# Optimization experiments

Measured on AMD Instinct MI355X. Metric: run time of the kernel, lower is better.

Reference implementation:

```python
import jax, jax.numpy as jnp
import numpy as np

D_MODEL = 512
N_HEADS = 8
D_K = D_MODEL // N_HEADS


def setup_inputs() -> dict:
    key = jax.random.key(0)
    ks = jax.random.split(key, 12)
    B, L = 2, 512
    s = 1.0 / np.sqrt(D_MODEL)
    sk = 1.0 / np.sqrt(D_K)
    return {
        "query": jax.random.normal(ks[0], (B, L, D_MODEL), jnp.float32),
        "key": jax.random.normal(ks[1], (B, L, D_MODEL), jnp.float32),
        "value": jax.random.normal(ks[2], (B, L, D_MODEL), jnp.float32),
        "Wq": jax.random.normal(ks[3], (D_MODEL, D_MODEL), jnp.float32) * s,
        "bq": jnp.zeros((D_MODEL,), jnp.float32),
        "Wk": jax.random.normal(ks[4], (D_MODEL, D_MODEL), jnp.float32) * s,
        "bk": jnp.zeros((D_MODEL,), jnp.float32),
        "Wv": jax.random.normal(ks[5], (D_MODEL, D_MODEL), jnp.float32) * s,
        "bv": jnp.zeros((D_MODEL,), jnp.float32),
        "Wo": jax.random.normal(ks[6], (D_MODEL, D_MODEL), jnp.float32) * s,
        "bo": jnp.zeros((D_MODEL,), jnp.float32),
        "Aq": jax.random.normal(ks[7], (D_K, D_K), jnp.float32) * sk,  # inner W_q (no bias)
        "Ak": jax.random.normal(ks[8], (D_K, D_K), jnp.float32) * sk,  # inner W_k (no bias)
        "av": jax.random.normal(ks[9], (D_K,), jnp.float32) * sk,      # inner v (d_k -> 1)
    }


def _split_heads(x):
    B, L, _ = x.shape
    return x.reshape(B, L, N_HEADS, D_K).transpose(0, 2, 1, 3)  # [B,H,L,dk]


def reference(query, key, value, Wq, bq, Wk, bk, Wv, bv, Wo, bo, Aq, Ak, av):
    # outer projections (torch Linear: x @ W.T + b)
    Q = _split_heads(query @ Wq.T + bq)   # [B,H,Lq,dk]
    K = _split_heads(key @ Wk.T + bk)     # [B,H,Lk,dk]
    V = _split_heads(value @ Wv.T + bv)   # [B,H,Lk,dk]
    # inner additive attention: e_ij = v^T tanh(Aq q_i + Ak k_j)
    qp = Q @ Aq.T                          # [B,H,Lq,dk]
    kp = K @ Ak.T                          # [B,H,Lk,dk]
    energy = jnp.tanh(qp[:, :, :, None, :] + kp[:, :, None, :, :])  # [B,H,Lq,Lk,dk]
    scores = jnp.einsum('bhqkd,d->bhqk', energy, av)
    attn = jax.nn.softmax(scores, axis=-1)  # dropout disabled (eval)
    out = jnp.einsum('bhqk,bhkd->bhqd', attn, V)  # [B,H,Lq,dk]
    B, _, Lq, _ = out.shape
    out = out.transpose(0, 2, 1, 3).reshape(B, Lq, D_MODEL)
    return out @ Wo.T + bo
```

## Files before the change

### kernel.cpp

```cpp
#include <hip/hip_runtime.h>

#define LOG2E 1.4426950408889634f

typedef __bf16 bf16x8 __attribute__((ext_vector_type(8)));
typedef float f32x4 __attribute__((ext_vector_type(4)));
typedef float f32x2 __attribute__((ext_vector_type(2)));

__device__ __forceinline__ unsigned short bfb(__bf16 b){
  union { __bf16 b; unsigned short u; } z; z.b = b; return z.u;
}
__device__ __forceinline__ void split8(const float* p, bf16x8& hi, bf16x8& lo){
  #pragma unroll
  for (int j = 0; j < 8; j++){
    float f = p[j];
    __bf16 h = (__bf16)f;
    hi[j] = h;
    lo[j] = (__bf16)(f - (float)h);
  }
}


__global__ __launch_bounds__(256) void prep_all(
    const float* __restrict__ Wq, const float* __restrict__ Aq,
    const float* __restrict__ Wk, const float* __restrict__ Ak,
    const float* __restrict__ bq, const float* __restrict__ bk,
    const float* __restrict__ av,
    const float* __restrict__ Wv, const float* __restrict__ Wo,
    unsigned short* __restrict__ W2qp, unsigned short* __restrict__ W2kp,
    unsigned short* __restrict__ Wvp,  unsigned short* __restrict__ Wop,
    float* __restrict__ b2q, float* __restrict__ b2k, float* __restrict__ av2g){
  if (blockIdx.x >= 256){
    if (blockIdx.x == 512){
      if (blockIdx.y == 0){
        #pragma unroll
        for (int rep = 0; rep < 2; rep++){
          int n = rep * 256 + threadIdx.x;
          int h = n >> 6, e = n & 63;
          float aq = 0.f, ak = 0.f;
          for (int c = 0; c < 64; c++){
            aq += Aq[e*64 + c] * bq[h*64 + c];
            ak += Ak[e*64 + c] * bk[h*64 + c];
          }
          b2q[n] = aq * (2.f * LOG2E);
          b2k[n] = ak * (2.f * LOG2E);
        }
      } else {
        if (threadIdx.x < 64) av2g[threadIdx.x] = -2.f * LOG2E * av[threadIdx.x];
      }
      return;
    }
    const float* src = blockIdx.y ? Wo : Wv;
    unsigned short* dst = blockIdx.y ? Wop : Wvp;
    int base = ((blockIdx.x - 256) * 256 + threadIdx.x) * 4;
    int n = base >> 9, k0 = base & 511;
    float4 v = *(const float4*)(src + base);
    ushort4 h, l;
    float f; __bf16 hb;
    f = v.x; hb = (__bf16)f; h.x = bfb(hb); l.x = bfb((__bf16)(f - (float)hb));
    f = v.y; hb = (__bf16)f; h.y = bfb(hb); l.y = bfb((__bf16)(f - (float)hb));
    f = v.z; hb = (__bf16)f; h.z = bfb(hb); l.z = bfb((__bf16)(f - (float)hb));
    f = v.w; hb = (__bf16)f; h.w = bfb(hb); l.w = bfb((__bf16)(f - (float)hb));
    int nt = n >> 4, ln = n & 15;
    int ks = k0 >> 5, q = (k0 & 31) >> 3, j0 = k0 & 7;
    size_t off = (size_t)((nt*16 + ks) * 2) * 512 + (q*16 + ln) * 8 + j0;
    *(ushort4*)(dst + off)       = h;
    *(ushort4*)(dst + off + 512) = l;
    return;
  }
  const float* W  = blockIdx.y ? Wk : Wq;
  const float* Am = blockIdx.y ? Ak : Aq;
  unsigned short* dst = blockIdx.y ? W2kp : W2qp;
  int idx = blockIdx.x * 256 + threadIdx.x;
  int n = idx >> 7;
  int k0 = (idx & 127) * 4;
  int h = n >> 6, e = n & 63;
  float4 acc = {0.f, 0.f, 0.f, 0.f};
  #pragma unroll 8
  for (int c = 0; c < 64; c++){
    float am = Am[e*64 + c];
    float4 wv = *(const float4*)(W + (size_t)(h*64 + c)*512 + k0);
    acc.x += am * wv.x;
    acc.y += am * wv.y;
    acc.z += am * wv.z;
    acc.w += am * wv.w;
  }
  int nt = n >> 4, ln = n & 15;
  int ks = k0 >> 5, q = (k0 & 31) >> 3, j0 = k0 & 7;
  size_t off = (size_t)((nt*16 + ks) * 2) * 512 + (q*16 + ln) * 8 + j0;
  ushort4 hh, ll;
  float f; __bf16 hb;
  f = acc.x * (2.f * LOG2E); hb = (__bf16)f; hh.x = bfb(hb); ll.x = bfb((__bf16)(f - (float)hb));
  f = acc.y * (2.f * LOG2E); hb = (__bf16)f; hh.y = bfb(hb); ll.y = bfb((__bf16)(f - (float)hb));
  f = acc.z * (2.f * LOG2E); hb = (__bf16)f; hh.z = bfb(hb); ll.z = bfb((__bf16)(f - (float)hb));
  f = acc.w * (2.f * LOG2E); hb = (__bf16)f; hh.w = bfb(hb); ll.w = bfb((__bf16)(f - (float)hb));
  *(ushort4*)(dst + off)       = hh;
  *(ushort4*)(dst + off + 512) = ll;
}

struct GemmBatch {
  const float* Af;
  const unsigned short* Bp;
  const float* bias;
  float* Cf;
  int transposed;
  int expout;
};
struct GemmArgs { GemmBatch g[3]; };

__global__ __launch_bounds__(256) void gemm_nk(GemmArgs ga){
  GemmBatch gb = ga.g[blockIdx.z];
  __shared__ float As[64 * 68];
  const int tid = threadIdx.x, lane = tid & 63, w = tid >> 6;
  const int l15 = lane & 15, quad = lane >> 4;
  const int m0  = blockIdx.x * 64;
  const int nt0 = blockIdx.y * 4;
  f32x4 ac0 = {0.f,0.f,0.f,0.f}, ac1 = ac0, ac2 = ac0, ac3 = ac0;

  const int sr = tid >> 2;
  const int sc = (tid & 3) * 16;
  const float* srcA = gb.Af + (size_t)(m0 + sr) * 512 + sc;
  float* dstA = &As[sr * 68 + sc];

  for (int kc = 0; kc < 8; kc++){
    __syncthreads();
    #pragma unroll
    for (int i = 0; i < 4; i++)
      *(f32x4*)(dstA + i*4) = *(const f32x4*)(srcA + kc*64 + i*4);
    __syncthreads();
    #pragma unroll
    for (int s = 0; s < 2; s++){
      int ks = kc * 2 + s;
      bf16x8 ah, al;
      split8(&As[(w*16 + l15) * 68 + s*32 + quad*8], ah, al);
      #pragma unroll
      for (int t = 0; t < 4; t++){
        const unsigned short* bp = gb.Bp + (size_t)(((nt0 + t)*16 + ks) * 2) * 512 + lane*8;
        bf16x8 bh = *(const bf16x8*)bp;
        bf16x8 bl = *(const bf16x8*)(bp + 512);
        f32x4& ac = (t==0)?ac0:(t==1)?ac1:(t==2)?ac2:ac3;
        ac = __builtin_amdgcn_mfma_f32_16x16x32_bf16(ah, bh, ac, 0, 0, 0);
        ac = __builtin_amdgcn_mfma_f32_16x16x32_bf16(al, bh, ac, 0, 0, 0);
        ac = __builtin_amdgcn_mfma_f32_16x16x32_bf16(ah, bl, ac, 0, 0, 0);
      }
    }
  }

  const int mrow = m0 + w * 16 + quad * 4;
  #pragma unroll
  for (int t = 0; t < 4; t++){
    f32x4 v = (t==0)?ac0:(t==1)?ac1:(t==2)?ac2:ac3;
    int n = nt0 * 16 + t * 16 + l15;
    float bs = gb.bias[n];
    #pragma unroll
    for (int r = 0; r < 4; r++){
      float val = v[r] + bs;
      if (gb.expout) val = __builtin_amdgcn_exp2f(val);
      int m2 = mrow + r;
      if (gb.transposed){
        gb.Cf[(size_t)(((m2 >> 9) * 8 + (n >> 6)) * 512 + (m2 & 511)) * 64 + (n & 63)] = val;
      } else {
        gb.Cf[(size_t)m2 * 512 + n] = val;
      }
    }
  }
}

__global__ __launch_bounds__(1024, 8) void attn_kernel(
    const float* __restrict__ eqQ, const float* __restrict__ ekp,
    const float* __restrict__ Vv, const float* __restrict__ av2g,
    float* __restrict__ Oh){
  __shared__ float bufA[64 * 130];
  __shared__ float bufB[64 * 130];
  __shared__ unsigned short pcb[2 * 16 * 136];
  __shared__ float dn[16];
  __shared__ float eqs[16 * 64];
  __shared__ float avs[64];
  float* cmb = bufA;

  const int tid = threadIdx.x, lane = tid & 63, w = tid >> 6;
  const int l15 = lane & 15, quad = lane >> 4;
  const int bh = blockIdx.y;
  const int i0 = blockIdx.x * 16;
  const size_t kbase = (size_t)(bh >> 3) * 512 * 512 + (size_t)(bh & 7) * 64;
  const int r0 = __builtin_amdgcn_readfirstlane(w);
  const int ntile = w & 3, kq = w >> 2;

  float den = 0.f;
  f32x4 Cacc = {0.f, 0.f, 0.f, 0.f};

  {
    eqs[w * 64 + lane] = eqQ[((size_t)bh * 512 + i0 + w) * 64 + lane];
    if (w == 0) avs[lane] = av2g[lane];
    #pragma unroll
    for (int m = 0; m < 4; m++){
      int i = w + 16 * m;
      float a = ekp[kbase + (size_t)(2*i    ) * 512 + lane];
      float b = ekp[kbase + (size_t)(2*i + 1) * 512 + lane];
      *(float2*)&bufA[lane * 130 + 2*i] = make_float2(a, b);
    }
  }
  __syncthreads();

  for (int c = 0; c < 4; c++){
    float va[4], vb[4], ka[4], kb[4];
    #pragma unroll
    for (int m = 0; m < 4; m++){
      int i = w + 16 * m;
      va[m] = Vv[kbase + (size_t)(c*128 + 2*i    ) * 512 + lane];
      vb[m] = Vv[kbase + (size_t)(c*128 + 2*i + 1) * 512 + lane];
    }
    if (c < 3){
      #pragma unroll
      for (int m = 0; m < 4; m++){
        int i = w + 16 * m;
        ka[m] = ekp[kbase + (size_t)((c+1)*128 + 2*i    ) * 512 + lane];
        kb[m] = ekp[kbase + (size_t)((c+1)*128 + 2*i + 1) * 512 + lane];
      }
    }
    f32x2 sacc = {0.f, 0.f};
    #pragma unroll 4
    for (int d = 0; d < 64; d += 4){
      f32x4 eq4 = *(const f32x4*)&eqs[r0 * 64 + d];
      f32x4 a4  = *(const f32x4*)&avs[d];
      f32x2 ek0 = *(const f32x2*)&bufA[(d  ) * 130 + 2 * lane];
      f32x2 ek1 = *(const f32x2*)&bufA[(d+1) * 130 + 2 * lane];
      f32x2 ek2 = *(const f32x2*)&bufA[(d+2) * 130 + 2 * lane];
      f32x2 ek3 = *(const f32x2*)&bufA[(d+3) * 130 + 2 * lane];
      f32x2 A = __builtin_elementwise_fma((f32x2){eq4[0], eq4[0]}, ek0, (f32x2){1.f, 1.f});
      f32x2 B = __builtin_elementwise_fma((f32x2){eq4[1], eq4[1]}, ek1, (f32x2){1.f, 1.f});
      f32x2 t = __builtin_elementwise_fma((f32x2){a4[1], a4[1]}, A, (f32x2){a4[0], a4[0]} * B);
      f32x2 dpr = A * B;
      f32x2 r;
      r.x = __builtin_amdgcn_rcpf(dpr.x);
      r.y = __builtin_amdgcn_rcpf(dpr.y);
      sacc = __builtin_elementwise_fma(t, r, sacc);
      f32x2 C = __builtin_elementwise_fma((f32x2){eq4[2], eq4[2]}, ek2, (f32x2){1.f, 1.f});
      f32x2 D = __builtin_elementwise_fma((f32x2){eq4[3], eq4[3]}, ek3, (f32x2){1.f, 1.f});
      f32x2 t2 = __builtin_elementwise_fma((f32x2){a4[3], a4[3]}, C, (f32x2){a4[2], a4[2]} * D);
      f32x2 dpr2 = C * D;
      f32x2 r2;
      r2.x = __builtin_amdgcn_rcpf(dpr2.x);
      r2.y = __builtin_amdgcn_rcpf(dpr2.y);
      sacc = __builtin_elementwise_fma(t2, r2, sacc);
    }
    float e0 = __builtin_amdgcn_exp2f(sacc.x);
    float e1 = __builtin_amdgcn_exp2f(sacc.y);
    den += e0 + e1;
    {
      __bf16 h0 = (__bf16)e0, h1 = (__bf16)e1;
      ushort2 hi = { bfb(h0), bfb(h1) };
      ushort2 lo = { bfb((__bf16)(e0 - (float)h0)), bfb((__bf16)(e1 - (float)h1)) };
      *(ushort2*)&pcb[(0*16 + r0) * 136 + 2*lane] = hi;
      *(ushort2*)&pcb[(1*16 + r0) * 136 + 2*lane] = lo;
    }
    #pragma unroll
    for (int m = 0; m < 4; m++){
      int i = w + 16 * m;
      *(float2*)&bufB[lane * 130 + 2*i] = make_float2(va[m], vb[m]);
    }
    __syncthreads();

    {
      int k0 = kq * 32 + quad * 8;
      bf16x8 ph = *(const bf16x8*)&pcb[(0*16 + l15) * 136 + k0];
      bf16x8 pl = *(const bf16x8*)&pcb[(1*16 + l15) * 136 + k0];
      const float* vp = &bufB[(ntile*16 + l15) * 130 + k0];
      bf16x8 vh, vl;
      #pragma unroll
      for (int j = 0; j < 8; j++){
        float f = vp[j];
        __bf16 h = (__bf16)f;
        vh[j] = h; vl[j] = (__bf16)(f - (float)h);
      }
      Cacc = __builtin_amdgcn_mfma_f32_16x16x32_bf16(ph, vh, Cacc, 0, 0, 0);
      Cacc = __builtin_amdgcn_mfma_f32_16x16x32_bf16(pl, vh, Cacc, 0, 0, 0);
      Cacc = __builtin_amdgcn_mfma_f32_16x16x32_bf16(ph, vl, Cacc, 0, 0, 0);
    }
    if (c < 3){
      #pragma unroll
      for (int m = 0; m < 4; m++){
        int i = w + 16 * m;
        *(float2*)&bufA[lane * 130 + 2*i] = make_float2(ka[m], kb[m]);
      }
    }
    __syncthreads();
  }

  #pragma unroll
  for (int off = 1; off < 64; off <<= 1)
    den += __shfl_xor(den, off, 64);
  if (lane == 0) dn[r0] = den;
  if (kq > 0){
    #pragma unroll
    for (int r = 0; r < 4; r++) cmb[(w - 4) * 256 + lane * 4 + r] = Cacc[r];
  }
  __syncthreads();
  if (kq == 0){
    #pragma unroll
    for (int r = 0; r < 4; r++){
      float cv = Cacc[r];
      #pragma unroll
      for (int j = 0; j < 3; j++) cv += cmb[(j*4 + ntile) * 256 + lane * 4 + r];
      int row = quad * 4 + r;
      int d = ntile * 16 + l15;
      Oh[kbase + (size_t)(i0 + row) * 512 + d] = cv / dn[row];
    }
  }
}

extern "C" void kernel_launch(void* const* d_in, const int* in_sizes, int n_in,
                              void* d_out, int out_size, void* d_ws, size_t ws_size,
                              hipStream_t stream){
  const float* q_in = (const float*)d_in[0];
  const float* k_in = (const float*)d_in[1];
  const float* v_in = (const float*)d_in[2];
  const float* Wq_  = (const float*)d_in[3];
  const float* bq_  = (const float*)d_in[4];
  const float* Wk_  = (const float*)d_in[5];
  const float* bk_  = (const float*)d_in[6];
  const float* Wv_  = (const float*)d_in[7];
  const float* bv_  = (const float*)d_in[8];
  const float* Wo_  = (const float*)d_in[9];
  const float* bo_  = (const float*)d_in[10];
  const float* Aq_  = (const float*)d_in[11];
  const float* Ak_  = (const float*)d_in[12];
  const float* av_  = (const float*)d_in[13];

  char* ws = (char*)d_ws;
  unsigned short* W2qp = (unsigned short*)(ws + 0);
  unsigned short* W2kp = (unsigned short*)(ws + 1048576);
  float* Oh = (float*)(ws + 0);
  unsigned short* Wvp = (unsigned short*)(ws + 2097152);
  unsigned short* Wop = (unsigned short*)(ws + 3145728);
  float* b2q  = (float*)(ws + 4194304);
  float* b2k  = (float*)(ws + 4196352);
  float* av2g = (float*)(ws + 4198400);
  float* eqQ  = (float*)(ws + 4198656);
  float* ekp  = (float*)(ws + 6295808);
  float* Vw   = (float*)(ws + 8392960);

  prep_all<<<dim3(513, 2, 1), 256, 0, stream>>>(Wq_, Aq_, Wk_, Ak_, bq_, bk_, av_,
                                                Wv_, Wo_,
                                                W2qp, W2kp, Wvp, Wop,
                                                b2q, b2k, av2g);

  GemmArgs ga;
  ga.g[0] = { q_in, W2qp, b2q, eqQ, 1, 1 };
  ga.g[1] = { k_in, W2kp, b2k, ekp, 0, 1 };
  ga.g[2] = { v_in, Wvp,  bv_, Vw,  0, 0 };
  gemm_nk<<<dim3(16, 8, 3), 256, 0, stream>>>(ga);

  attn_kernel<<<dim3(32, 16, 1), 1024, 0, stream>>>(eqQ, ekp, Vw, av2g, Oh);

  GemmArgs go;
  go.g[0] = { Oh, Wop, bo_, (float*)d_out, 0, 0 };
  go.g[1] = go.g[0];
  go.g[2] = go.g[0];
  gemm_nk<<<dim3(16, 8, 1), 256, 0, stream>>>(go);
}
```

Measured before the change: 161.3 us.

## Pre-split GEMM A operands to bf16 hi/lo and halve GEMM M-tile

The fp32 activations (q, k, v inputs and the attention output) are now split into bf16 hi/lo arrays ahead of time, in extra prep_all blocks or in the attention epilogue. The GEMM then loads them directly into shared memory instead of re-splitting in every block. The GEMM tile shrinks to 32 rows with a 2x2 warp layout, doubling grid size for more parallelism, and adds register prefetch of the next A chunk. The cost is extra global traffic writing and reading the hi/lo copies, plus more redundant B-operand loads per block.

```diff
diff --git a/kernel.cpp b/kernel.cpp
--- a/kernel.cpp
+++ b/kernel.cpp
@@ -5,18 +5,10 @@
 typedef __bf16 bf16x8 __attribute__((ext_vector_type(8)));
 typedef float f32x4 __attribute__((ext_vector_type(4)));
 typedef float f32x2 __attribute__((ext_vector_type(2)));
+typedef unsigned short u16x8 __attribute__((ext_vector_type(8)));
 
 __device__ __forceinline__ unsigned short bfb(__bf16 b){
   union { __bf16 b; unsigned short u; } z; z.b = b; return z.u;
-}
-__device__ __forceinline__ void split8(const float* p, bf16x8& hi, bf16x8& lo){
-  #pragma unroll
-  for (int j = 0; j < 8; j++){
-    float f = p[j];
-    __bf16 h = (__bf16)f;
-    hi[j] = h;
-    lo[j] = (__bf16)(f - (float)h);
-  }
 }
 
 
@@ -26,9 +18,36 @@
     const float* __restrict__ bq, const float* __restrict__ bk,
     const float* __restrict__ av,
     const float* __restrict__ Wv, const float* __restrict__ Wo,
+    const float* __restrict__ Qin, const float* __restrict__ Kin,
+    const float* __restrict__ Vin,
     unsigned short* __restrict__ W2qp, unsigned short* __restrict__ W2kp,
     unsigned short* __restrict__ Wvp,  unsigned short* __restrict__ Wop,
+    unsigned short* __restrict__ qhi, unsigned short* __restrict__ qlo,
+    unsigned short* __restrict__ khi, unsigned short* __restrict__ klo,
+    unsigned short* __restrict__ vhi, unsigned short* __restrict__ vlo,
     float* __restrict__ b2q, float* __restrict__ b2k, float* __restrict__ av2g){
+  if (blockIdx.x >= 513){
+    if (blockIdx.y) return;
+    int j = blockIdx.x - 513;
+    const float* src; unsigned short *dh, *dl;
+    if (j < 256){ src = Qin; dh = qhi; dl = qlo; }
+    else if (j < 512){ src = Kin; dh = khi; dl = klo; j -= 256; }
+    else { src = Vin; dh = vhi; dl = vlo; j -= 512; }
+    int base = (j * 256 + threadIdx.x) * 8;
+    f32x4 v0 = *(const f32x4*)(src + base);
+    f32x4 v1 = *(const f32x4*)(src + base + 4);
+    u16x8 hh, ll;
+    #pragma unroll
+    for (int t = 0; t < 8; t++){
+      float f = (t < 4) ? v0[t] : v1[t - 4];
+      __bf16 hb = (__bf16)f;
+      hh[t] = bfb(hb);
+      ll[t] = bfb((__bf16)(f - (float)hb));
+    }
+    *(u16x8*)(dh + base) = hh;
+    *(u16x8*)(dl + base) = ll;
+    return;
+  }
   if (blockIdx.x >= 256){
     if (blockIdx.x == 512){
       if (blockIdx.y == 0){
@@ -98,7 +117,8 @@
 }
 
 struct GemmBatch {
-  const float* Af;
+  const unsigned short* Ahi;
+  const unsigned short* Alo;
   const unsigned short* Bp;
   const float* bias;
   float* Cf;
@@ -109,35 +129,47 @@
 
 __global__ __launch_bounds__(256) void gemm_nk(GemmArgs ga){
   GemmBatch gb = ga.g[blockIdx.z];
-  __shared__ float As[64 * 68];
+  __shared__ unsigned short AhiS[32 * 72];
+  __shared__ unsigned short AloS[32 * 72];
   const int tid = threadIdx.x, lane = tid & 63, w = tid >> 6;
   const int l15 = lane & 15, quad = lane >> 4;
-  const int m0  = blockIdx.x * 64;
+  const int m0  = blockIdx.x * 32;
   const int nt0 = blockIdx.y * 4;
-  f32x4 ac0 = {0.f,0.f,0.f,0.f}, ac1 = ac0, ac2 = ac0, ac3 = ac0;
-
-  const int sr = tid >> 2;
-  const int sc = (tid & 3) * 16;
-  const float* srcA = gb.Af + (size_t)(m0 + sr) * 512 + sc;
-  float* dstA = &As[sr * 68 + sc];
+  const int wr = w >> 1, wc = w & 1;
+  f32x4 ac0 = {0.f,0.f,0.f,0.f}, ac1 = ac0;
+
+  const int srow = tid >> 3;
+  const int scol = (tid & 7) * 8;
+  const unsigned short* srcH = gb.Ahi + (size_t)(m0 + srow) * 512 + scol;
+  const unsigned short* srcL = gb.Alo + (size_t)(m0 + srow) * 512 + scol;
+  unsigned short* dstH = &AhiS[srow * 72 + scol];
+  unsigned short* dstL = &AloS[srow * 72 + scol];
+  u16x8 ph = *(const u16x8*)srcH;
+  u16x8 pl = *(const u16x8*)srcL;
+
+  const int arow = (wr * 16 + l15) * 72;
 
   for (int kc = 0; kc < 8; kc++){
     __syncthreads();
-    #pragma unroll
-    for (int i = 0; i < 4; i++)
-      *(f32x4*)(dstA + i*4) = *(const f32x4*)(srcA + kc*64 + i*4);
+    *(u16x8*)dstH = ph;
+    *(u16x8*)dstL = pl;
+    if (kc < 7){
+      ph = *(const u16x8*)(srcH + (kc + 1) * 64);
+      pl = *(const u16x8*)(srcL + (kc + 1) * 64);
+    }
     __syncthreads();
     #pragma unroll
     for (int s = 0; s < 2; s++){
       int ks = kc * 2 + s;
-      bf16x8 ah, al;
-      split8(&As[(w*16 + l15) * 68 + s*32 + quad*8], ah, al);
+      bf16x8 ah = *(const bf16x8*)&AhiS[arow + s*32 + quad*8];
+      bf16x8 al = *(const bf16x8*)&AloS[arow + s*32 + quad*8];
       #pragma unroll
-      for (int t = 0; t < 4; t++){
-        const unsigned short* bp = gb.Bp + (size_t)(((nt0 + t)*16 + ks) * 2) * 512 + lane*8;
+      for (int t = 0; t < 2; t++){
+        int nt = nt0 + wc*2 + t;
+        const unsigned short* bp = gb.Bp + (size_t)((nt*16 + ks) * 2) * 512 + lane*8;
         bf16x8 bh = *(const bf16x8*)bp;
         bf16x8 bl = *(const bf16x8*)(bp + 512);
-        f32x4& ac = (t==0)?ac0:(t==1)?ac1:(t==2)?ac2:ac3;
+        f32x4& ac = t ? ac1 : ac0;
         ac = __builtin_amdgcn_mfma_f32_16x16x32_bf16(ah, bh, ac, 0, 0, 0);
         ac = __builtin_amdgcn_mfma_f32_16x16x32_bf16(al, bh, ac, 0, 0, 0);
         ac = __builtin_amdgcn_mfma_f32_16x16x32_bf16(ah, bl, ac, 0, 0, 0);
@@ -145,11 +177,11 @@
     }
   }
 
-  const int mrow = m0 + w * 16 + quad * 4;
+  const int mrow = m0 + wr * 16 + quad * 4;
   #pragma unroll
-  for (int t = 0; t < 4; t++){
-    f32x4 v = (t==0)?ac0:(t==1)?ac1:(t==2)?ac2:ac3;
-    int n = nt0 * 16 + t * 16 + l15;
+  for (int t = 0; t < 2; t++){
+    f32x4 v = t ? ac1 : ac0;
+    int n = nt0*16 + wc*32 + t*16 + l15;
     float bs = gb.bias[n];
     #pragma unroll
     for (int r = 0; r < 4; r++){
@@ -168,7 +200,7 @@
 __global__ __launch_bounds__(1024, 8) void attn_kernel(
     const float* __restrict__ eqQ, const float* __restrict__ ekp,
     const float* __restrict__ Vv, const float* __restrict__ av2g,
-    float* __restrict__ Oh){
+    unsigned short* __restrict__ Ohhi, unsigned short* __restrict__ Ohlo){
   __shared__ float bufA[64 * 130];
   __shared__ float bufB[64 * 130];
   __shared__ unsigned short pcb[2 * 16 * 136];
@@ -303,7 +335,11 @@
       for (int j = 0; j < 3; j++) cv += cmb[(j*4 + ntile) * 256 + lane * 4 + r];
       int row = quad * 4 + r;
       int d = ntile * 16 + l15;
-      Oh[kbase + (size_t)(i0 + row) * 512 + d] = cv / dn[row];
+      float val = cv / dn[row];
+      __bf16 hb = (__bf16)val;
+      size_t oi = kbase + (size_t)(i0 + row) * 512 + d;
+      Ohhi[oi] = bfb(hb);
+      Ohlo[oi] = bfb((__bf16)(val - (float)hb));
     }
   }
 }
@@ -329,32 +365,40 @@
   char* ws = (char*)d_ws;
   unsigned short* W2qp = (unsigned short*)(ws + 0);
   unsigned short* W2kp = (unsigned short*)(ws + 1048576);
-  float* Oh = (float*)(ws + 0);
-  unsigned short* Wvp = (unsigned short*)(ws + 2097152);
-  unsigned short* Wop = (unsigned short*)(ws + 3145728);
+  unsigned short* Ohhi = (unsigned short*)(ws + 0);
+  unsigned short* Ohlo = (unsigned short*)(ws + 1048576);
+  unsigned short* Wvp  = (unsigned short*)(ws + 2097152);
+  unsigned short* Wop  = (unsigned short*)(ws + 3145728);
   float* b2q  = (float*)(ws + 4194304);
   float* b2k  = (float*)(ws + 4196352);
   float* av2g = (float*)(ws + 4198400);
   float* eqQ  = (float*)(ws + 4198656);
   float* ekp  = (float*)(ws + 6295808);
   float* Vw   = (float*)(ws + 8392960);
-
-  prep_all<<<dim3(513, 2, 1), 256, 0, stream>>>(Wq_, Aq_, Wk_, Ak_, bq_, bk_, av_,
-                                                Wv_, Wo_,
-                                                W2qp, W2kp, Wvp, Wop,
-                                                b2q, b2k, av2g);
+  unsigned short* qhi = (unsigned short*)(ws + 10490112);
+  unsigned short* qlo = (unsigned short*)(ws + 11538688);
+  unsigned short* khi = (unsigned short*)(ws + 12587264);
+  unsigned short* klo = (unsigned short*)(ws + 13635840);
+  unsigned short* vhi = (unsigned short*)(ws + 14684416);
+  unsigned short* vlo = (unsigned short*)(ws + 15732992);
+
+  prep_all<<<dim3(1281, 2, 1), 256, 0, stream>>>(Wq_, Aq_, Wk_, Ak_, bq_, bk_, av_,
+                                                 Wv_, Wo_, q_in, k_in, v_in,
+                                                 W2qp, W2kp, Wvp, Wop,
+                                                 qhi, qlo, khi, klo, vhi, vlo,
+                                                 b2q, b2k, av2g);
 
   GemmArgs ga;
-  ga.g[0] = { q_in, W2qp, b2q, eqQ, 1, 1 };
-  ga.g[1] = { k_in, W2kp, b2k, ekp, 0, 1 };
-  ga.g[2] = { v_in, Wvp,  bv_, Vw,  0, 0 };
-  gemm_nk<<<dim3(16, 8, 3), 256, 0, stream>>>(ga);
-
-  attn_kernel<<<dim3(32, 16, 1), 1024, 0, stream>>>(eqQ, ekp, Vw, av2g, Oh);
+  ga.g[0] = { qhi, qlo, W2qp, b2q, eqQ, 1, 1 };
+  ga.g[1] = { khi, klo, W2kp, b2k, ekp, 0, 1 };
+  ga.g[2] = { vhi, vlo, Wvp,  bv_, Vw,  0, 0 };
+  gemm_nk<<<dim3(32, 8, 3), 256, 0, stream>>>(ga);
+
+  attn_kernel<<<dim3(32, 16, 1), 1024, 0, stream>>>(eqQ, ekp, Vw, av2g, Ohhi, Ohlo);
 
   GemmArgs go;
-  go.g[0] = { Oh, Wop, bo_, (float*)d_out, 0, 0 };
+  go.g[0] = { Ohhi, Ohlo, Wop, bo_, (float*)d_out, 0, 0 };
   go.g[1] = go.g[0];
   go.g[2] = go.g[0];
-  gemm_nk<<<dim3(16, 8, 1), 256, 0, stream>>>(go);
+  gemm_nk<<<dim3(32, 8, 1), 256, 0, stream>>>(go);
 }
```

New measurement: 151.8 us. -5.9%, faster.
